# Performance work log

Hardware: AMD Instinct MI355X
Metric: run time of the kernel (lower is better)

Reference implementation:

```python
import jax, jax.numpy as jnp
import numpy as np

POOL_SIZES = [(5, 10), (3, 6), (2, 4)]
P_VALUE = 1e-8
EVAL_T = 0.03


def _pool_up(k, p0, p1):
    # avg_pool2d with kernel=stride=(H/p0, W/p1), padding 0 (exact divisibility),
    # followed by repeat_interleave upsampling back to (B,H,W,D).
    B, H, W, D = k.shape
    kh, kw = H // p0, W // p1
    pooled = k.reshape(B, p0, kh, p1, kw, D).mean(axis=(2, 4))  # (B,p0,p1,D)
    up = jnp.broadcast_to(pooled[:, :, None, :, None, :], (B, p0, kh, p1, kw, D))
    return up.reshape(B, H, W, D)


def setup_inputs() -> dict:
    key = jax.random.key(0)
    ks = jax.random.split(key, 7)
    B, H, W, D = 64, 30, 60, 64
    x = jax.random.normal(ks[0], (B, H, W, D), dtype=jnp.float32)
    qk_w = jax.random.normal(ks[1], (2 * D, D), dtype=jnp.float32) * 0.02
    qk_b = jax.random.normal(ks[2], (2 * D,), dtype=jnp.float32) * 0.02
    score_w = jax.random.normal(ks[3], (1, 3), dtype=jnp.float32) * 0.5
    score_b = jax.random.normal(ks[4], (1,), dtype=jnp.float32) * 0.5
    noise_x = jax.random.uniform(ks[5], (B, H * W, 1), dtype=jnp.float32)
    noise_r = jax.random.uniform(ks[6], (B, H * W, 1), dtype=jnp.float32)
    return {"x": x, "qk_w": qk_w, "qk_b": qk_b, "score_w": score_w,
            "score_b": score_b, "noise_x": noise_x, "noise_r": noise_r}


def reference(x, qk_w, qk_b, score_w, score_b, noise_x, noise_r):
    B, H, W, D = x.shape
    scale = D ** (-0.5)
    qk = x @ qk_w.T + qk_b                      # (B,H,W,2D)
    q, k = qk[..., :D], qk[..., D:]             # (B,H,W,D)
    # attn[:,0,1:] only uses row 0 (original q) vs pooled k columns 1..3.
    scores = jnp.stack(
        [jnp.sum(q * _pool_up(k, p0, p1), axis=-1) for (p0, p1) in POOL_SIZES],
        axis=-1) * scale                        # (B,H,W,3)
    attn = scores @ score_w.T + score_b         # (B,H,W,1)
    attn = attn.reshape(B, H * W, 1)
    attn_soft = jax.nn.sigmoid(attn)
    # gumbel-sigmoid (eval mode, T = 0.03)
    gx = jnp.log(attn_soft + P_VALUE)
    gr = jnp.log(1.0 - attn_soft + P_VALUE)
    nx = -jnp.log(-jnp.log(noise_x + P_VALUE) + P_VALUE)
    nr = -jnp.log(-jnp.log(noise_r + P_VALUE) + P_VALUE)
    gx = (gx + nx) / (EVAL_T + P_VALUE)
    gr = (gr + nr) / (EVAL_T + P_VALUE)
    logits = jnp.concatenate([gx, gr], axis=-1)  # (B,HW,2)
    mask = jax.nn.softmax(logits, axis=-1)[..., 0:1]  # (B,HW,1)
    return mask
```

## Files before the change

kernel.cpp:

```cpp
#include <hip/hip_runtime.h>
#include <math.h>

#define BB 64
#define HH 30
#define WW 60
#define DD 64
#define NPIX 1800
#define NREG 76

__constant__ int c_rowband[HH] = {0,0,0,0,0,0, 1,1,1,1, 2,2, 3,3,3, 4,4,4, 5,5, 6,6,6,6, 7,7,7,7,7,7};
__constant__ int c_colband[WW] = {0,0,0,0,0,0, 1,1,1,1, 2,2, 3,3,3, 4,4,4, 5,5, 6,6,6,6, 7,7,7,7,7,7,
                                  8,8,8,8,8,8, 9,9,9,9, 10,10, 11,11,11, 12,12,12, 13,13, 14,14,14,14, 15,15,15,15,15,15};
__constant__ int c_s0col[16] = {0,1,1,2,2,3,3,4,5,6,6,7,7,8,8,9};
__constant__ int c_s1col[16] = {0,0,1,1,1,1,2,2,3,3,4,4,4,4,5,5};
__constant__ int c_s0row[8] = {0,1,1,2,2,3,3,4};
__constant__ int c_s1row[8] = {0,0,1,1,1,1,2,2};

__global__ __launch_bounds__(256) void ka_pool(
    const float* __restrict__ x, float* __restrict__ psum)
{
    const int b = blockIdx.x / HH;
    const int h = blockIdx.x % HH;
    const int t = threadIdx.x;
    const int j = t & 63;
    const int g = t >> 6;

    const float* xrow = x + ((size_t)(b * NPIX + h * WW) + g * 15) * DD;
    float v[15];
#pragma unroll
    for (int i = 0; i < 15; ++i) v[i] = xrow[i * DD + j];

    float a0, a1, a2, a3;
    if ((g & 1) == 0) {
        a0 = ((v[0]+v[1])+(v[2]+v[3]))+(v[4]+v[5]);
        a1 = (v[6]+v[7])+(v[8]+v[9]);
        a2 = v[10]+v[11];
        a3 = (v[12]+v[13])+v[14];
    } else {
        a0 = (v[0]+v[1])+v[2];
        a1 = v[3]+v[4];
        a2 = (v[5]+v[6])+(v[7]+v[8]);
        a3 = ((v[9]+v[10])+(v[11]+v[12]))+(v[13]+v[14]);
    }

    const float s0m = a1 + a2;
    const float s10 = a0 + a1;
    const float s11 = a2 + a3;
    const float s2  = s10 + s11;

    const int r0 = (h / 6) * 10;
    const int r1 = 50 + (h / 10) * 6;
    const int r2 = 68 + (h / 15) * 4;
    const int c0a = c_s0col[4*g], c0b = c_s0col[4*g+1], c0c = c_s0col[4*g+3];
    const int c1a = c_s1col[4*g], c1b = c_s1col[4*g+2];

    float* pb = psum + (size_t)b * NREG * 64 + j;
    atomicAdd(pb + (r0 + c0a) * 64, a0);
    atomicAdd(pb + (r0 + c0b) * 64, s0m);
    atomicAdd(pb + (r0 + c0c) * 64, a3);
    atomicAdd(pb + (r1 + c1a) * 64, s10);
    atomicAdd(pb + (r1 + c1b) * 64, s11);
    atomicAdd(pb + (r2 + g) * 64, s2);
}

__global__ __launch_bounds__(256) void kb_cells(
    const float* __restrict__ qk_w, const float* __restrict__ qk_b,
    const float* __restrict__ score_w, const float* __restrict__ score_b,
    const float* __restrict__ psum, float* __restrict__ G, float* __restrict__ cc)
{
    __shared__ float R[NREG * 64];
    __shared__ float WQ[64 * 64];
    __shared__ float WKT[64 * 65];
    __shared__ float XCOMB[32 * 64];
    __shared__ float M[32 * 64];
    __shared__ float BQ[64];

    const int b = blockIdx.x >> 2;
    const int cell0 = (blockIdx.x & 3) * 32;
    const int t = threadIdx.x;
    const int lane = t & 63;
    const int g = t >> 6;

    for (int i = t; i < NREG * 64; i += 256) R[i] = psum[(size_t)b * NREG * 64 + i];
    for (int i = t; i < 4096; i += 256) {
        const int jj = i >> 6, d = i & 63;
        WQ[i] = qk_w[i];
        WKT[d * 65 + jj] = qk_w[(64 + jj) * 64 + d];
    }
    if (t < 64) BQ[t] = qk_b[t];
    __syncthreads();

    const float w0 = score_w[0] * (1.0f / 36.0f);
    const float w1 = score_w[1] * (1.0f / 100.0f);
    const float w2 = score_w[2] * (1.0f / 225.0f);
    const float wsum = score_w[0] + score_w[1] + score_w[2];

    for (int i = t; i < 32 * 64; i += 256) {
        const int lcell = i >> 6, d = i & 63;
        const int cell = cell0 + lcell;
        const int rb = cell >> 4, cb = cell & 15;
        const int r0 = 10 * c_s0row[rb] + c_s0col[cb];
        const int r1 = 50 + 6 * c_s1row[rb] + c_s1col[cb];
        const int r2 = 68 + 4 * (rb >> 2) + (cb >> 2);
        XCOMB[i] = w0 * R[r0 * 64 + d] + w1 * R[r1 * 64 + d] + w2 * R[r2 * 64 + d];
    }
    __syncthreads();

    {
        float wkreg[64];
#pragma unroll
        for (int d = 0; d < 64; ++d) wkreg[d] = WKT[d * 65 + lane];
        const float bkv = qk_b[64 + lane];
        for (int cidx = 0; cidx < 8; ++cidx) {
            const int lcell = g * 8 + cidx;
            const float4* xc = (const float4*)(XCOMB + lcell * 64);
            float acc = 0.f;
#pragma unroll
            for (int q = 0; q < 16; ++q) {
                const float4 m4 = xc[q];
                acc += m4.x * wkreg[4*q] + m4.y * wkreg[4*q+1]
                     + m4.z * wkreg[4*q+2] + m4.w * wkreg[4*q+3];
            }
            M[lcell * 64 + lane] = acc + wsum * bkv;
        }
    }
    __syncthreads();

    {
        float wqreg[64];
#pragma unroll
        for (int jj = 0; jj < 64; ++jj) wqreg[jj] = WQ[jj * 64 + lane];
        const float scl = 0.125f;
        const float sb = score_b[0];
        const float4* bq4 = (const float4*)BQ;
        for (int cidx = 0; cidx < 8; ++cidx) {
            const int lcell = g * 8 + cidx;
            const float4* m4p = (const float4*)(M + lcell * 64);
            float acc = 0.f, cacc = 0.f;
#pragma unroll
            for (int q = 0; q < 16; ++q) {
                const float4 m4 = m4p[q];
                const float4 b4 = bq4[q];
                acc  += m4.x * wqreg[4*q] + m4.y * wqreg[4*q+1]
                      + m4.z * wqreg[4*q+2] + m4.w * wqreg[4*q+3];
                cacc += m4.x * b4.x + m4.y * b4.y + m4.z * b4.z + m4.w * b4.w;
            }
            const int cell = cell0 + lcell;
            G[(size_t)b * 8192 + cell * 64 + lane] = scl * acc;
            if (lane == 0) cc[b * 128 + cell] = scl * cacc + sb;
        }
    }
}

__global__ __launch_bounds__(256) void kc_mask(
    const float* __restrict__ x, const float* __restrict__ G,
    const float* __restrict__ cc, const float* __restrict__ noise_x,
    const float* __restrict__ noise_r, float* __restrict__ out)
{
    __shared__ float Grow[1024];
    __shared__ float crow[16];
    __shared__ float attnv[64];
    __shared__ int cbt[64];

    const int b = blockIdx.x / HH;
    const int h = blockIdx.x % HH;
    const int t = threadIdx.x;
    const int lane = t & 63;
    const int g = t >> 6;
    const int rb = c_rowband[h];

    ((float4*)Grow)[t] = ((const float4*)(G + (size_t)b * 8192 + rb * 1024))[t];
    if (t < 16) crow[t] = cc[b * 128 + rb * 16 + t];
    if (t < 60) cbt[t] = c_colband[t];
    __syncthreads();

    const float4* x4 = (const float4*)(x + (size_t)(b * NPIX + h * WW) * DD);
    const int f = lane & 15;
    const int pg = lane >> 4;
#pragma unroll
    for (int i = 0; i < 4; ++i) {
        const int pl = i * 4 + pg;
        if (pl < 15) {
            const int p = g * 15 + pl;
            const int cb = cbt[p];
            const float4 xv = x4[p * 16 + f];
            const float4 gv = ((const float4*)Grow)[cb * 16 + f];
            float s = xv.x * gv.x + xv.y * gv.y + xv.z * gv.z + xv.w * gv.w;
            s += __shfl_xor(s, 1, 64);
            s += __shfl_xor(s, 2, 64);
            s += __shfl_xor(s, 4, 64);
            s += __shfl_xor(s, 8, 64);
            if (f == 0) attnv[p] = s + crow[cb];
        }
    }
    __syncthreads();

    if (t < 60) {
        const int pix = b * NPIX + h * WW + t;
        const float a = attnv[t];
        const float s  = 1.0f / (1.0f + expf(-a));
        const float gx = logf(s + 1e-8f);
        const float gr = logf(1.0f - s + 1e-8f);
        const float ux = noise_x[pix];
        const float ur = noise_r[pix];
        const float nx = -logf(-logf(ux + 1e-8f) + 1e-8f);
        const float nr = -logf(-logf(ur + 1e-8f) + 1e-8f);
        const float INV_T = 1.0f / (0.03f + 1e-8f);
        const float A = (gx + nx) * INV_T;
        const float R = (gr + nr) * INV_T;
        out[pix] = 1.0f / (1.0f + expf(R - A));
    }
}

extern "C" void kernel_launch(void* const* d_in, const int* in_sizes, int n_in,
                              void* d_out, int out_size, void* d_ws, size_t ws_size,
                              hipStream_t stream)
{
    const float* x       = (const float*)d_in[0];
    const float* qk_w    = (const float*)d_in[1];
    const float* qk_b    = (const float*)d_in[2];
    const float* score_w = (const float*)d_in[3];
    const float* score_b = (const float*)d_in[4];
    const float* noise_x = (const float*)d_in[5];
    const float* noise_r = (const float*)d_in[6];
    float* out = (float*)d_out;

    float* psum = (float*)d_ws;
    float* G    = psum + (size_t)BB * NREG * 64;
    float* cc   = G + (size_t)BB * 128 * 64;

    hipMemsetAsync(psum, 0, (size_t)BB * NREG * 64 * sizeof(float), stream);
    ka_pool<<<BB * HH, 256, 0, stream>>>(x, psum);
    kb_cells<<<BB * 4, 256, 0, stream>>>(qk_w, qk_b, score_w, score_b, psum, G, cc);
    kc_mask<<<BB * HH, 256, 0, stream>>>(x, G, cc, noise_x, noise_r, out);
}
```

Measured before the change: 112.5 us.

## Fuse cell projection into mask kernel via precomputed Wq^T Wk product

Replaces the atomic pooling, the per-batch two-stage qk projection kernel and the memset with two kernels. The first computes per-band pooled partial sums without atomics, and extra blocks precompute the combined weight matrix E = Wq^T Wk plus the bias vectors. The second kernel rebuilds each row band's pooled cells from the band sums and applies a single 64x64 product with E per block, then computes the mask. This cuts a launch, the memset and the atomics, but every mask block now repeats a small matmul and loads the 16KB E matrix.

```diff
diff --git a/kernel.cpp b/kernel.cpp
--- a/kernel.cpp
+++ b/kernel.cpp
@@ -6,172 +6,180 @@
 #define WW 60
 #define DD 64
 #define NPIX 1800
-#define NREG 76
-
-__constant__ int c_rowband[HH] = {0,0,0,0,0,0, 1,1,1,1, 2,2, 3,3,3, 4,4,4, 5,5, 6,6,6,6, 7,7,7,7,7,7};
+
 __constant__ int c_colband[WW] = {0,0,0,0,0,0, 1,1,1,1, 2,2, 3,3,3, 4,4,4, 5,5, 6,6,6,6, 7,7,7,7,7,7,
                                   8,8,8,8,8,8, 9,9,9,9, 10,10, 11,11,11, 12,12,12, 13,13, 14,14,14,14, 15,15,15,15,15,15};
+__constant__ int c_band_start[8] = {0,6,10,12,15,18,20,24};
+__constant__ int c_band_cnt[8]   = {6,4,2,3,3,2,4,6};
+__constant__ int c_first[20] = {0,1,3,5,7,8,9,11,13,15, 0,2,6,8,10,14, 0,4,8,12};
+__constant__ int c_cnt[20]   = {1,2,2,2,1,1,2,2,2,1,   2,4,2,2,4,2,   4,4,4,4};
 __constant__ int c_s0col[16] = {0,1,1,2,2,3,3,4,5,6,6,7,7,8,8,9};
 __constant__ int c_s1col[16] = {0,0,1,1,1,1,2,2,3,3,4,4,4,4,5,5};
-__constant__ int c_s0row[8] = {0,1,1,2,2,3,3,4};
-__constant__ int c_s1row[8] = {0,0,1,1,1,1,2,2};
-
-__global__ __launch_bounds__(256) void ka_pool(
-    const float* __restrict__ x, float* __restrict__ psum)
+__constant__ int c_s0bf[5] = {0,1,3,5,7};
+__constant__ int c_s0bc[5] = {1,2,2,2,1};
+__constant__ int c_s1bf[3] = {0,2,6};
+__constant__ int c_s1bc[3] = {2,4,2};
+__constant__ int c_s2bf[2] = {0,4};
+
+__global__ __launch_bounds__(256) void k1_pool_E(
+    const float* __restrict__ x, const float* __restrict__ qk_w,
+    const float* __restrict__ qk_b, float* __restrict__ bandsums,
+    float* __restrict__ ET_ws, float* __restrict__ u_ws,
+    float* __restrict__ v_ws, float* __restrict__ s_ws)
 {
-    const int b = blockIdx.x / HH;
-    const int h = blockIdx.x % HH;
     const int t = threadIdx.x;
+
+    if (blockIdx.x >= 512) {
+        const int e = blockIdx.x - 512;
+        if (t < 64) {
+            float acc = 0.f;
+#pragma unroll 8
+            for (int jj = 0; jj < 64; ++jj)
+                acc += qk_w[jj * 64 + t] * qk_w[(64 + e) * 64 + jj];
+            acc = 0.f;
+#pragma unroll 8
+            for (int jj = 0; jj < 64; ++jj)
+                acc += qk_w[jj * 64 + t] * qk_w[(64 + jj) * 64 + e];
+            ET_ws[e * 64 + t] = acc;
+        } else if (e == 0 && t >= 64 && t < 128) {
+            const int d = t - 64;
+            float acc = 0.f;
+            for (int jj = 0; jj < 64; ++jj) acc += qk_w[jj * 64 + d] * qk_b[64 + jj];
+            u_ws[d] = acc;
+        } else if (e == 0 && t >= 128 && t < 192) {
+            const int e2 = t - 128;
+            float acc = 0.f;
+            for (int jj = 0; jj < 64; ++jj) acc += qk_w[(64 + jj) * 64 + e2] * qk_b[jj];
+            v_ws[e2] = acc;
+        } else if (e == 0 && t == 192) {
+            float acc = 0.f;
+            for (int jj = 0; jj < 64; ++jj) acc += qk_b[jj] * qk_b[64 + jj];
+            s_ws[0] = acc;
+        }
+        return;
+    }
+
+    __shared__ float pools[16 * 64];
+    const int b = blockIdx.x >> 3;
+    const int band = blockIdx.x & 7;
     const int j = t & 63;
     const int g = t >> 6;
-
-    const float* xrow = x + ((size_t)(b * NPIX + h * WW) + g * 15) * DD;
-    float v[15];
-#pragma unroll
-    for (int i = 0; i < 15; ++i) v[i] = xrow[i * DD + j];
-
-    float a0, a1, a2, a3;
-    if ((g & 1) == 0) {
-        a0 = ((v[0]+v[1])+(v[2]+v[3]))+(v[4]+v[5]);
-        a1 = (v[6]+v[7])+(v[8]+v[9]);
-        a2 = v[10]+v[11];
-        a3 = (v[12]+v[13])+v[14];
-    } else {
-        a0 = (v[0]+v[1])+v[2];
-        a1 = v[3]+v[4];
-        a2 = (v[5]+v[6])+(v[7]+v[8]);
-        a3 = ((v[9]+v[10])+(v[11]+v[12]))+(v[13]+v[14]);
-    }
-
-    const float s0m = a1 + a2;
-    const float s10 = a0 + a1;
-    const float s11 = a2 + a3;
-    const float s2  = s10 + s11;
-
-    const int r0 = (h / 6) * 10;
-    const int r1 = 50 + (h / 10) * 6;
-    const int r2 = 68 + (h / 15) * 4;
-    const int c0a = c_s0col[4*g], c0b = c_s0col[4*g+1], c0c = c_s0col[4*g+3];
-    const int c1a = c_s1col[4*g], c1b = c_s1col[4*g+2];
-
-    float* pb = psum + (size_t)b * NREG * 64 + j;
-    atomicAdd(pb + (r0 + c0a) * 64, a0);
-    atomicAdd(pb + (r0 + c0b) * 64, s0m);
-    atomicAdd(pb + (r0 + c0c) * 64, a3);
-    atomicAdd(pb + (r1 + c1a) * 64, s10);
-    atomicAdd(pb + (r1 + c1b) * 64, s11);
-    atomicAdd(pb + (r2 + g) * 64, s2);
+    const int h0 = c_band_start[band];
+    const int nr = c_band_cnt[band];
+
+    float A0 = 0.f, A1 = 0.f, A2 = 0.f, A3 = 0.f;
+    for (int r = 0; r < nr; ++r) {
+        const float* xrow = x + ((size_t)(b * NPIX + (h0 + r) * WW) + g * 15) * DD;
+        float v[15];
+#pragma unroll
+        for (int i = 0; i < 15; ++i) v[i] = xrow[i * DD + j];
+        if ((g & 1) == 0) {
+            A0 += ((v[0]+v[1])+(v[2]+v[3]))+(v[4]+v[5]);
+            A1 += (v[6]+v[7])+(v[8]+v[9]);
+            A2 += v[10]+v[11];
+            A3 += (v[12]+v[13])+v[14];
+        } else {
+            A0 += (v[0]+v[1])+v[2];
+            A1 += v[3]+v[4];
+            A2 += (v[5]+v[6])+(v[7]+v[8]);
+            A3 += ((v[9]+v[10])+(v[11]+v[12]))+(v[13]+v[14]);
+        }
+    }
+    pools[(g * 4 + 0) * 64 + j] = A0;
+    pools[(g * 4 + 1) * 64 + j] = A1;
+    pools[(g * 4 + 2) * 64 + j] = A2;
+    pools[(g * 4 + 3) * 64 + j] = A3;
+    __syncthreads();
+
+    float* outp = bandsums + (((size_t)b * 8 + band) * 20) * 64;
+    for (int i = t; i < 20 * 64; i += 256) {
+        const int c = i >> 6, d = i & 63;
+        const int f = c_first[c], n = c_cnt[c];
+        float s = 0.f;
+        for (int q = 0; q < n; ++q) s += pools[(f + q) * 64 + d];
+        outp[i] = s;
+    }
 }
 
-__global__ __launch_bounds__(256) void kb_cells(
-    const float* __restrict__ qk_w, const float* __restrict__ qk_b,
-    const float* __restrict__ score_w, const float* __restrict__ score_b,
-    const float* __restrict__ psum, float* __restrict__ G, float* __restrict__ cc)
+__global__ __launch_bounds__(256) void k2_mask(
+    const float* __restrict__ x, const float* __restrict__ score_w,
+    const float* __restrict__ score_b, const float* __restrict__ bandsums,
+    const float* __restrict__ ET_ws, const float* __restrict__ u_ws,
+    const float* __restrict__ v_ws, const float* __restrict__ s_ws,
+    const float* __restrict__ noise_x, const float* __restrict__ noise_r,
+    float* __restrict__ out)
 {
-    __shared__ float R[NREG * 64];
-    __shared__ float WQ[64 * 64];
-    __shared__ float WKT[64 * 65];
-    __shared__ float XCOMB[32 * 64];
-    __shared__ float M[32 * 64];
-    __shared__ float BQ[64];
-
-    const int b = blockIdx.x >> 2;
-    const int cell0 = (blockIdx.x & 3) * 32;
-    const int t = threadIdx.x;
-    const int lane = t & 63;
-    const int g = t >> 6;
-
-    for (int i = t; i < NREG * 64; i += 256) R[i] = psum[(size_t)b * NREG * 64 + i];
-    for (int i = t; i < 4096; i += 256) {
-        const int jj = i >> 6, d = i & 63;
-        WQ[i] = qk_w[i];
-        WKT[d * 65 + jj] = qk_w[(64 + jj) * 64 + d];
-    }
-    if (t < 64) BQ[t] = qk_b[t];
-    __syncthreads();
-
-    const float w0 = score_w[0] * (1.0f / 36.0f);
-    const float w1 = score_w[1] * (1.0f / 100.0f);
-    const float w2 = score_w[2] * (1.0f / 225.0f);
-    const float wsum = score_w[0] + score_w[1] + score_w[2];
-
-    for (int i = t; i < 32 * 64; i += 256) {
-        const int lcell = i >> 6, d = i & 63;
-        const int cell = cell0 + lcell;
-        const int rb = cell >> 4, cb = cell & 15;
-        const int r0 = 10 * c_s0row[rb] + c_s0col[cb];
-        const int r1 = 50 + 6 * c_s1row[rb] + c_s1col[cb];
-        const int r2 = 68 + 4 * (rb >> 2) + (cb >> 2);
-        XCOMB[i] = w0 * R[r0 * 64 + d] + w1 * R[r1 * 64 + d] + w2 * R[r2 * 64 + d];
-    }
-    __syncthreads();
-
-    {
-        float wkreg[64];
-#pragma unroll
-        for (int d = 0; d < 64; ++d) wkreg[d] = WKT[d * 65 + lane];
-        const float bkv = qk_b[64 + lane];
-        for (int cidx = 0; cidx < 8; ++cidx) {
-            const int lcell = g * 8 + cidx;
-            const float4* xc = (const float4*)(XCOMB + lcell * 64);
-            float acc = 0.f;
-#pragma unroll
-            for (int q = 0; q < 16; ++q) {
-                const float4 m4 = xc[q];
-                acc += m4.x * wkreg[4*q] + m4.y * wkreg[4*q+1]
-                     + m4.z * wkreg[4*q+2] + m4.w * wkreg[4*q+3];
-            }
-            M[lcell * 64 + lane] = acc + wsum * bkv;
-        }
-    }
-    __syncthreads();
-
-    {
-        float wqreg[64];
-#pragma unroll
-        for (int jj = 0; jj < 64; ++jj) wqreg[jj] = WQ[jj * 64 + lane];
-        const float scl = 0.125f;
-        const float sb = score_b[0];
-        const float4* bq4 = (const float4*)BQ;
-        for (int cidx = 0; cidx < 8; ++cidx) {
-            const int lcell = g * 8 + cidx;
-            const float4* m4p = (const float4*)(M + lcell * 64);
-            float acc = 0.f, cacc = 0.f;
-#pragma unroll
-            for (int q = 0; q < 16; ++q) {
-                const float4 m4 = m4p[q];
-                const float4 b4 = bq4[q];
-                acc  += m4.x * wqreg[4*q] + m4.y * wqreg[4*q+1]
-                      + m4.z * wqreg[4*q+2] + m4.w * wqreg[4*q+3];
-                cacc += m4.x * b4.x + m4.y * b4.y + m4.z * b4.z + m4.w * b4.w;
-            }
-            const int cell = cell0 + lcell;
-            G[(size_t)b * 8192 + cell * 64 + lane] = scl * acc;
-            if (lane == 0) cc[b * 128 + cell] = scl * cacc + sb;
-        }
-    }
-}
-
-__global__ __launch_bounds__(256) void kc_mask(
-    const float* __restrict__ x, const float* __restrict__ G,
-    const float* __restrict__ cc, const float* __restrict__ noise_x,
-    const float* __restrict__ noise_r, float* __restrict__ out)
-{
-    __shared__ float Grow[1024];
+    __shared__ float ET[64 * 64];
+    __shared__ float R[20 * 64];
+    __shared__ float XC[16 * 64];
+    __shared__ float Gl[16 * 64];
+    __shared__ float ul[64], vl[64];
     __shared__ float crow[16];
     __shared__ float attnv[64];
-    __shared__ int cbt[64];
 
     const int b = blockIdx.x / HH;
     const int h = blockIdx.x % HH;
     const int t = threadIdx.x;
     const int lane = t & 63;
     const int g = t >> 6;
-    const int rb = c_rowband[h];
-
-    ((float4*)Grow)[t] = ((const float4*)(G + (size_t)b * 8192 + rb * 1024))[t];
-    if (t < 16) crow[t] = cc[b * 128 + rb * 16 + t];
-    if (t < 60) cbt[t] = c_colband[t];
+
+    for (int i = t; i < 4096; i += 256) ET[i] = ET_ws[i];
+    if (t < 64) ul[t] = u_ws[t];
+    else if (t < 128) vl[t - 64] = v_ws[t - 64];
+
+    const int s0r = h / 6, s1r = h / 10, s2r = h / 15;
+    const float* bs = bandsums + (size_t)b * 8 * 20 * 64;
+    for (int i = t; i < 20 * 64; i += 256) {
+        const int c = i >> 6;
+        int f, n;
+        if (c < 10)      { f = c_s0bf[s0r]; n = c_s0bc[s0r]; }
+        else if (c < 16) { f = c_s1bf[s1r]; n = c_s1bc[s1r]; }
+        else             { f = c_s2bf[s2r]; n = 4; }
+        float s = 0.f;
+        for (int q = 0; q < n; ++q) s += bs[((size_t)(f + q) * 20) * 64 + i];
+        R[i] = s;
+    }
+    __syncthreads();
+
+    const float w0n = score_w[0] * (1.0f / 36.0f);
+    const float w1n = score_w[1] * (1.0f / 100.0f);
+    const float w2n = score_w[2] * (1.0f / 225.0f);
+    for (int i = t; i < 16 * 64; i += 256) {
+        const int cb = i >> 6, d = i & 63;
+        XC[i] = w0n * R[c_s0col[cb] * 64 + d]
+              + w1n * R[(10 + c_s1col[cb]) * 64 + d]
+              + w2n * R[(16 + (cb >> 2)) * 64 + d];
+    }
+    __syncthreads();
+
+    {
+        const float wsum = score_w[0] + score_w[1] + score_w[2];
+        const float sv = s_ws[0];
+        const float sb = score_b[0];
+        float xfrag[4], acc[4];
+#pragma unroll
+        for (int ci = 0; ci < 4; ++ci) {
+            xfrag[ci] = XC[(g * 4 + ci) * 64 + lane];
+            acc[ci] = 0.f;
+        }
+#pragma unroll 16
+        for (int e = 0; e < 64; ++e) {
+            const float ecol = ET[e * 64 + lane];
+#pragma unroll
+            for (int ci = 0; ci < 4; ++ci)
+                acc[ci] += ecol * __shfl(xfrag[ci], e, 64);
+        }
+#pragma unroll
+        for (int ci = 0; ci < 4; ++ci) {
+            const int cg = g * 4 + ci;
+            Gl[cg * 64 + lane] = 0.125f * (acc[ci] + wsum * ul[lane]);
+            float pv = vl[lane] * xfrag[ci];
+            pv += __shfl_xor(pv, 1, 64);  pv += __shfl_xor(pv, 2, 64);
+            pv += __shfl_xor(pv, 4, 64);  pv += __shfl_xor(pv, 8, 64);
+            pv += __shfl_xor(pv, 16, 64); pv += __shfl_xor(pv, 32, 64);
+            if (lane == 0) crow[cg] = 0.125f * (pv + wsum * sv) + sb;
+        }
+    }
     __syncthreads();
 
     const float4* x4 = (const float4*)(x + (size_t)(b * NPIX + h * WW) * DD);
@@ -182,9 +190,9 @@
         const int pl = i * 4 + pg;
         if (pl < 15) {
             const int p = g * 15 + pl;
-            const int cb = cbt[p];
+            const int cb = c_colband[p];
             const float4 xv = x4[p * 16 + f];
-            const float4 gv = ((const float4*)Grow)[cb * 16 + f];
+            const float4 gv = ((const float4*)Gl)[cb * 16 + f];
             float s = xv.x * gv.x + xv.y * gv.y + xv.z * gv.z + xv.w * gv.w;
             s += __shfl_xor(s, 1, 64);
             s += __shfl_xor(s, 2, 64);
@@ -198,17 +206,17 @@
     if (t < 60) {
         const int pix = b * NPIX + h * WW + t;
         const float a = attnv[t];
-        const float s  = 1.0f / (1.0f + expf(-a));
-        const float gx = logf(s + 1e-8f);
-        const float gr = logf(1.0f - s + 1e-8f);
+        const float sg = 1.0f / (1.0f + expf(-a));
+        const float gx = logf(sg + 1e-8f);
+        const float gr = logf(1.0f - sg + 1e-8f);
         const float ux = noise_x[pix];
         const float ur = noise_r[pix];
         const float nx = -logf(-logf(ux + 1e-8f) + 1e-8f);
         const float nr = -logf(-logf(ur + 1e-8f) + 1e-8f);
         const float INV_T = 1.0f / (0.03f + 1e-8f);
         const float A = (gx + nx) * INV_T;
-        const float R = (gr + nr) * INV_T;
-        out[pix] = 1.0f / (1.0f + expf(R - A));
+        const float Rr = (gr + nr) * INV_T;
+        out[pix] = 1.0f / (1.0f + expf(Rr - A));
     }
 }
 
@@ -225,12 +233,13 @@
     const float* noise_r = (const float*)d_in[6];
     float* out = (float*)d_out;
 
-    float* psum = (float*)d_ws;
-    float* G    = psum + (size_t)BB * NREG * 64;
-    float* cc   = G + (size_t)BB * 128 * 64;
-
-    hipMemsetAsync(psum, 0, (size_t)BB * NREG * 64 * sizeof(float), stream);
-    ka_pool<<<BB * HH, 256, 0, stream>>>(x, psum);
-    kb_cells<<<BB * 4, 256, 0, stream>>>(qk_w, qk_b, score_w, score_b, psum, G, cc);
-    kc_mask<<<BB * HH, 256, 0, stream>>>(x, G, cc, noise_x, noise_r, out);
+    float* bandsums = (float*)d_ws;
+    float* ET_ws = bandsums + 655360;
+    float* u_ws  = ET_ws + 4096;
+    float* v_ws  = u_ws + 64;
+    float* s_ws  = v_ws + 64;
+
+    k1_pool_E<<<576, 256, 0, stream>>>(x, qk_w, qk_b, bandsums, ET_ws, u_ws, v_ws, s_ws);
+    k2_mask<<<BB * HH, 256, 0, stream>>>(x, score_w, score_b, bandsums, ET_ws, u_ws, v_ws, s_ws,
+                                         noise_x, noise_r, out);
 }
```

After: 128.7 us. 14.4% more time.

## Precompute Wq^T Wk product once and collapse two-stage cell matmul into one

Applied to the files above, without the earlier changes.

Extra blocks appended to the pooling kernel precompute the 64x64 product of the query and key weights, plus bias cross-terms u, v and s, into workspace. The cell kernel then needs a single 64x64 matvec per cell against this fused matrix instead of projecting to K and then through WQ. It also runs on 512 blocks instead of 256 and stages only the pooled rows it needs rather than the full region table. In exchange the pooling launch gains 64 serial-dot-product blocks, and the reassociated sums may change floating-point rounding slightly.

```diff
diff --git a/kernel.cpp b/kernel.cpp
--- a/kernel.cpp
+++ b/kernel.cpp
@@ -17,11 +17,41 @@
 __constant__ int c_s1row[8] = {0,0,1,1,1,1,2,2};
 
 __global__ __launch_bounds__(256) void ka_pool(
-    const float* __restrict__ x, float* __restrict__ psum)
-{
+    const float* __restrict__ x, const float* __restrict__ qk_w,
+    const float* __restrict__ qk_b, float* __restrict__ psum,
+    float* __restrict__ ET_ws, float* __restrict__ u_ws,
+    float* __restrict__ v_ws, float* __restrict__ s_ws)
+{
+    const int t = threadIdx.x;
+
+    if (blockIdx.x >= BB * HH) {
+        const int e = blockIdx.x - BB * HH;
+        if (t < 64) {
+            float acc = 0.f;
+#pragma unroll 8
+            for (int jj = 0; jj < 64; ++jj)
+                acc += qk_w[jj * 64 + t] * qk_w[(64 + jj) * 64 + e];
+            ET_ws[e * 64 + t] = acc;
+        } else if (e == 0 && t >= 64 && t < 128) {
+            const int d = t - 64;
+            float acc = 0.f;
+            for (int jj = 0; jj < 64; ++jj) acc += qk_w[jj * 64 + d] * qk_b[64 + jj];
+            u_ws[d] = acc;
+        } else if (e == 0 && t >= 128 && t < 192) {
+            const int e2 = t - 128;
+            float acc = 0.f;
+            for (int jj = 0; jj < 64; ++jj) acc += qk_w[(64 + jj) * 64 + e2] * qk_b[jj];
+            v_ws[e2] = acc;
+        } else if (e == 0 && t == 192) {
+            float acc = 0.f;
+            for (int jj = 0; jj < 64; ++jj) acc += qk_b[jj] * qk_b[64 + jj];
+            s_ws[0] = acc;
+        }
+        return;
+    }
+
     const int b = blockIdx.x / HH;
     const int h = blockIdx.x % HH;
-    const int t = threadIdx.x;
     const int j = t & 63;
     const int g = t >> 6;
 
@@ -63,92 +93,68 @@
     atomicAdd(pb + (r2 + g) * 64, s2);
 }
 
-__global__ __launch_bounds__(256) void kb_cells(
-    const float* __restrict__ qk_w, const float* __restrict__ qk_b,
+__global__ __launch_bounds__(256) void kb_G(
     const float* __restrict__ score_w, const float* __restrict__ score_b,
-    const float* __restrict__ psum, float* __restrict__ G, float* __restrict__ cc)
-{
-    __shared__ float R[NREG * 64];
-    __shared__ float WQ[64 * 64];
-    __shared__ float WKT[64 * 65];
-    __shared__ float XCOMB[32 * 64];
-    __shared__ float M[32 * 64];
-    __shared__ float BQ[64];
-
-    const int b = blockIdx.x >> 2;
-    const int cell0 = (blockIdx.x & 3) * 32;
+    const float* __restrict__ psum, const float* __restrict__ ET_ws,
+    const float* __restrict__ u_ws, const float* __restrict__ v_ws,
+    const float* __restrict__ s_ws, float* __restrict__ G, float* __restrict__ cc)
+{
+    __shared__ float ETs[4096];
+    __shared__ float XC[16 * 64];
+    __shared__ float ul[64], vl[64];
+
+    const int b = blockIdx.x >> 3;
+    const int rb = blockIdx.x & 7;
     const int t = threadIdx.x;
     const int lane = t & 63;
     const int g = t >> 6;
 
-    for (int i = t; i < NREG * 64; i += 256) R[i] = psum[(size_t)b * NREG * 64 + i];
-    for (int i = t; i < 4096; i += 256) {
-        const int jj = i >> 6, d = i & 63;
-        WQ[i] = qk_w[i];
-        WKT[d * 65 + jj] = qk_w[(64 + jj) * 64 + d];
-    }
-    if (t < 64) BQ[t] = qk_b[t];
+    for (int i = t; i < 4096; i += 256) ETs[i] = ET_ws[i];
+    if (t < 64) ul[t] = u_ws[t];
+    else if (t < 128) vl[t - 64] = v_ws[t - 64];
+
+    const float w0n = score_w[0] * (1.0f / 36.0f);
+    const float w1n = score_w[1] * (1.0f / 100.0f);
+    const float w2n = score_w[2] * (1.0f / 225.0f);
+    const float* pb = psum + (size_t)b * NREG * 64;
+    const int r0 = 10 * c_s0row[rb];
+    const int r1 = 50 + 6 * c_s1row[rb];
+    const int r2 = 68 + 4 * (rb >> 2);
+    for (int i = t; i < 16 * 64; i += 256) {
+        const int cb = i >> 6, d = i & 63;
+        XC[i] = w0n * pb[(r0 + c_s0col[cb]) * 64 + d]
+              + w1n * pb[(r1 + c_s1col[cb]) * 64 + d]
+              + w2n * pb[(r2 + (cb >> 2)) * 64 + d];
+    }
     __syncthreads();
 
-    const float w0 = score_w[0] * (1.0f / 36.0f);
-    const float w1 = score_w[1] * (1.0f / 100.0f);
-    const float w2 = score_w[2] * (1.0f / 225.0f);
+    float et[64];
+#pragma unroll
+    for (int e = 0; e < 64; ++e) et[e] = ETs[e * 64 + lane];
+
     const float wsum = score_w[0] + score_w[1] + score_w[2];
-
-    for (int i = t; i < 32 * 64; i += 256) {
-        const int lcell = i >> 6, d = i & 63;
-        const int cell = cell0 + lcell;
-        const int rb = cell >> 4, cb = cell & 15;
-        const int r0 = 10 * c_s0row[rb] + c_s0col[cb];
-        const int r1 = 50 + 6 * c_s1row[rb] + c_s1col[cb];
-        const int r2 = 68 + 4 * (rb >> 2) + (cb >> 2);
-        XCOMB[i] = w0 * R[r0 * 64 + d] + w1 * R[r1 * 64 + d] + w2 * R[r2 * 64 + d];
-    }
-    __syncthreads();
-
-    {
-        float wkreg[64];
-#pragma unroll
-        for (int d = 0; d < 64; ++d) wkreg[d] = WKT[d * 65 + lane];
-        const float bkv = qk_b[64 + lane];
-        for (int cidx = 0; cidx < 8; ++cidx) {
-            const int lcell = g * 8 + cidx;
-            const float4* xc = (const float4*)(XCOMB + lcell * 64);
-            float acc = 0.f;
-#pragma unroll
-            for (int q = 0; q < 16; ++q) {
-                const float4 m4 = xc[q];
-                acc += m4.x * wkreg[4*q] + m4.y * wkreg[4*q+1]
-                     + m4.z * wkreg[4*q+2] + m4.w * wkreg[4*q+3];
-            }
-            M[lcell * 64 + lane] = acc + wsum * bkv;
+    const float sv = s_ws[0];
+    const float sb = score_b[0];
+    const float uval = ul[lane];
+    const float vval = vl[lane];
+
+#pragma unroll
+    for (int ci = 0; ci < 4; ++ci) {
+        const int cb = g * 4 + ci;
+        const float4* xc4 = (const float4*)(XC + cb * 64);
+        float acc = 0.f;
+#pragma unroll
+        for (int q = 0; q < 16; ++q) {
+            const float4 xv = xc4[q];
+            acc += xv.x * et[4*q] + xv.y * et[4*q+1] + xv.z * et[4*q+2] + xv.w * et[4*q+3];
         }
-    }
-    __syncthreads();
-
-    {
-        float wqreg[64];
-#pragma unroll
-        for (int jj = 0; jj < 64; ++jj) wqreg[jj] = WQ[jj * 64 + lane];
-        const float scl = 0.125f;
-        const float sb = score_b[0];
-        const float4* bq4 = (const float4*)BQ;
-        for (int cidx = 0; cidx < 8; ++cidx) {
-            const int lcell = g * 8 + cidx;
-            const float4* m4p = (const float4*)(M + lcell * 64);
-            float acc = 0.f, cacc = 0.f;
-#pragma unroll
-            for (int q = 0; q < 16; ++q) {
-                const float4 m4 = m4p[q];
-                const float4 b4 = bq4[q];
-                acc  += m4.x * wqreg[4*q] + m4.y * wqreg[4*q+1]
-                      + m4.z * wqreg[4*q+2] + m4.w * wqreg[4*q+3];
-                cacc += m4.x * b4.x + m4.y * b4.y + m4.z * b4.z + m4.w * b4.w;
-            }
-            const int cell = cell0 + lcell;
-            G[(size_t)b * 8192 + cell * 64 + lane] = scl * acc;
-            if (lane == 0) cc[b * 128 + cell] = scl * cacc + sb;
-        }
+        G[(size_t)b * 8192 + rb * 1024 + cb * 64 + lane] = 0.125f * (acc + wsum * uval);
+
+        float pv = vval * XC[cb * 64 + lane];
+        pv += __shfl_xor(pv, 1, 64);  pv += __shfl_xor(pv, 2, 64);
+        pv += __shfl_xor(pv, 4, 64);  pv += __shfl_xor(pv, 8, 64);
+        pv += __shfl_xor(pv, 16, 64); pv += __shfl_xor(pv, 32, 64);
+        if (lane == 0) cc[b * 128 + rb * 16 + cb] = 0.125f * (pv + wsum * sv) + sb;
     }
 }
 
@@ -198,9 +204,9 @@
     if (t < 60) {
         const int pix = b * NPIX + h * WW + t;
         const float a = attnv[t];
-        const float s  = 1.0f / (1.0f + expf(-a));
-        const float gx = logf(s + 1e-8f);
-        const float gr = logf(1.0f - s + 1e-8f);
+        const float sg = 1.0f / (1.0f + expf(-a));
+        const float gx = logf(sg + 1e-8f);
+        const float gr = logf(1.0f - sg + 1e-8f);
         const float ux = noise_x[pix];
         const float ur = noise_r[pix];
         const float nx = -logf(-logf(ux + 1e-8f) + 1e-8f);
@@ -225,12 +231,16 @@
     const float* noise_r = (const float*)d_in[6];
     float* out = (float*)d_out;
 
-    float* psum = (float*)d_ws;
-    float* G    = psum + (size_t)BB * NREG * 64;
-    float* cc   = G + (size_t)BB * 128 * 64;
+    float* psum  = (float*)d_ws;
+    float* G     = psum + (size_t)BB * NREG * 64;
+    float* cc    = G + (size_t)BB * 128 * 64;
+    float* ET_ws = cc + BB * 128;
+    float* u_ws  = ET_ws + 4096;
+    float* v_ws  = u_ws + 64;
+    float* s_ws  = v_ws + 64;
 
     hipMemsetAsync(psum, 0, (size_t)BB * NREG * 64 * sizeof(float), stream);
-    ka_pool<<<BB * HH, 256, 0, stream>>>(x, psum);
-    kb_cells<<<BB * 4, 256, 0, stream>>>(qk_w, qk_b, score_w, score_b, psum, G, cc);
+    ka_pool<<<BB * HH + 64, 256, 0, stream>>>(x, qk_w, qk_b, psum, ET_ws, u_ws, v_ws, s_ws);
+    kb_G<<<BB * 8, 256, 0, stream>>>(score_w, score_b, psum, ET_ws, u_ws, v_ws, s_ws, G, cc);
     kc_mask<<<BB * HH, 256, 0, stream>>>(x, G, cc, noise_x, noise_r, out);
 }
```

Measured after the change: 109.0 us. -3.2%, faster.
